# Kernel tuning notes

Measured on AMD Instinct MI355X. Metric: run time of the kernel, lower is better.

The kernel has to match this reference:

```python
import jax, jax.numpy as jnp
import numpy as np

B, T, IN, H, OUT = 512, 1024, 16, 128, 1


def _lstm_layer(x_tbd, W_ih, W_hh, b_ih, b_hh):
    """Single LSTM layer, PyTorch gate order (i, f, g, o).
    x_tbd: [T, B, D_in] -> returns [T, B, H]."""
    Tn, Bn = x_tbd.shape[0], x_tbd.shape[1]
    # Precompute input contribution for all timesteps: [T, B, 4H]
    gx = jnp.einsum('tbd,gd->tbg', x_tbd, W_ih) + b_ih + b_hh
    h0 = jnp.zeros((Bn, H), x_tbd.dtype)
    c0 = jnp.zeros((Bn, H), x_tbd.dtype)

    def step(carry, gx_t):
        h, c = carry
        gates = gx_t + h @ W_hh.T  # [B, 4H]
        i = jax.nn.sigmoid(gates[:, 0 * H:1 * H])
        f = jax.nn.sigmoid(gates[:, 1 * H:2 * H])
        g = jnp.tanh(gates[:, 2 * H:3 * H])
        o = jax.nn.sigmoid(gates[:, 3 * H:4 * H])
        c = f * c + i * g
        h = o * jnp.tanh(c)
        return (h, c), h

    _, hs = jax.lax.scan(step, (h0, c0), gx)
    return hs  # [T, B, H]


def setup_inputs() -> dict:
    key = jax.random.key(0)
    ks = jax.random.split(key, 12)
    s = 1.0 / np.sqrt(H)  # PyTorch LSTM init scale
    return {
        'x': jax.random.normal(ks[0], (B, T, IN), jnp.float32),
        'W_ih0': jax.random.uniform(ks[1], (4 * H, IN), jnp.float32, -s, s),
        'W_hh0': jax.random.uniform(ks[2], (4 * H, H), jnp.float32, -s, s),
        'b_ih0': jax.random.uniform(ks[3], (4 * H,), jnp.float32, -s, s),
        'b_hh0': jax.random.uniform(ks[4], (4 * H,), jnp.float32, -s, s),
        'W_ih1': jax.random.uniform(ks[5], (4 * H, H), jnp.float32, -s, s),
        'W_hh1': jax.random.uniform(ks[6], (4 * H, H), jnp.float32, -s, s),
        'b_ih1': jax.random.uniform(ks[7], (4 * H,), jnp.float32, -s, s),
        'b_hh1': jax.random.uniform(ks[8], (4 * H,), jnp.float32, -s, s),
        'W_fc': jax.random.uniform(ks[9], (OUT, H), jnp.float32, -s, s),
        'b_fc': jax.random.uniform(ks[10], (OUT,), jnp.float32, -s, s),
    }


def reference(x, W_ih0, W_hh0, b_ih0, b_hh0, W_ih1, W_hh1, b_ih1, b_hh1, W_fc, b_fc):
    x_tbd = jnp.transpose(x, (1, 0, 2))  # [T, B, IN]
    h1 = _lstm_layer(x_tbd, W_ih0, W_hh0, b_ih0, b_hh0)  # [T, B, H]
    h2 = _lstm_layer(h1, W_ih1, W_hh1, b_ih1, b_hh1)     # [T, B, H]
    out = jnp.transpose(h2, (1, 0, 2))  # [B, T, H]
    out = jax.nn.relu(out)
    out = out @ W_fc.T + b_fc  # [B, T, 1]
    out = jax.nn.relu(out)
    return out
```

## Files before the change

### kernel.cpp

```cpp
#include <hip/hip_runtime.h>

#define T_SEQ  1024
#define NBATCH 512
#define IN_DIM 16
#define HDIM   128
#define G4     (4 * HDIM)
#define TC     64
#define NCHUNK (T_SEQ / TC)
#define NWGH   128

typedef unsigned short ushort_t;
typedef __attribute__((ext_vector_type(8))) _Float16 f16x8;
typedef __attribute__((ext_vector_type(4))) float f32x4;

#define MFMA16(a, b, c) __builtin_amdgcn_mfma_f32_16x16x32_f16((a), (b), (c), 0, 0, 0)

__device__ __forceinline__ float sigf(float x) {
  return __builtin_amdgcn_rcpf(1.0f + __expf(-x));
}
__device__ __forceinline__ float tanhf_fast(float x) {
  return 1.0f - 2.0f * __builtin_amdgcn_rcpf(1.0f + __expf(2.0f * x));
}
__device__ __forceinline__ ushort_t f16_bits(float f) {
  const _Float16 h = (_Float16)f;
  return __builtin_bit_cast(unsigned short, h);
}
__device__ __forceinline__ void split_f16(float f, ushort_t* hi, ushort_t* lo) {
  const _Float16 h = (_Float16)f;
  *hi = __builtin_bit_cast(unsigned short, h);
  const _Float16 l = (_Float16)(f - (float)h);
  *lo = __builtin_bit_cast(unsigned short, l);
}
__device__ __forceinline__ void bar_lds() {
  asm volatile("s_waitcnt lgkmcnt(0)\n\ts_barrier" ::: "memory");
}

__global__ __launch_bounds__(256) void prep_weights(
    const float* __restrict__ Whh0, const float* __restrict__ Whh1,
    const float* __restrict__ Wih0, const float* __restrict__ Wih1,
    ushort_t* __restrict__ w0h, ushort_t* __restrict__ w0l,
    ushort_t* __restrict__ w1h, ushort_t* __restrict__ w1l,
    ushort_t* __restrict__ wxh, ushort_t* __restrict__ wxl,
    ushort_t* __restrict__ wi1h, ushort_t* __restrict__ wi1l)
{
  const int idx = blockIdx.x * 256 + threadIdx.x;
  if (idx < 512 * HDIM) {
    split_f16(Whh0[idx], &w0h[idx], &w0l[idx]);
    split_f16(Whh1[idx], &w1h[idx], &w1l[idx]);
    split_f16(Wih1[idx], &wi1h[idx], &wi1l[idx]);
  }
  if (idx < 512 * 32) {
    const int g = idx >> 5, k = idx & 31;
    const float f = (k < IN_DIM) ? Wih0[g * IN_DIM + k] : 0.0f;
    split_f16(f, &wxh[idx], &wxl[idx]);
  }
}

struct L0LDS {
  __align__(16) ushort_t hfA[4][144];
  __align__(16) ushort_t hfB[4][144];
  __align__(16) ushort_t xlds[4][TC][32];
  __align__(16) float gx0s[8 * 4 * 128 * 4];
};
struct L1LDS {
  __align__(16) ushort_t hfA[4][144];
  __align__(16) ushort_t hfB[4][144];
  __align__(16) ushort_t h2l[TC][4][136];
  __align__(16) float wfl[HDIM];
};

__global__ __launch_bounds__(512, 2) void lstm_pipe(
    const float* __restrict__ x,
    const ushort_t* __restrict__ w0h,
    const ushort_t* __restrict__ wxh, const ushort_t* __restrict__ wxl,
    const float* __restrict__ bih0, const float* __restrict__ bhh0,
    const ushort_t* __restrict__ wi1h,
    const ushort_t* __restrict__ w1h,
    const float* __restrict__ bih1, const float* __restrict__ bhh1,
    const float* __restrict__ Wfc, const float* __restrict__ bfc,
    float* __restrict__ out,
    float* __restrict__ h1s, float* __restrict__ c1s,
    float* __restrict__ h2s, float* __restrict__ c2s,
    ushort_t* __restrict__ h1buf,
    float* __restrict__ gx1buf,
    int ch)
{
  const int tid  = threadIdx.x;
  const int lane = tid & 63;
  const int wv   = tid >> 6;
  const int row  = lane & 15;
  const int kq   = lane >> 4;
  const int bq   = row >> 2;
  const int j    = wv * 16 + row;

  constexpr size_t POOL =
      sizeof(L0LDS) > sizeof(L1LDS) ? sizeof(L0LDS) : sizeof(L1LDS);
  __shared__ __align__(16) char pool[POOL];

  if (blockIdx.x < NWGH) {
    if (ch >= NCHUNK) return;
    L0LDS& S = *(L0LDS*)pool;
    const int w  = blockIdx.x;
    const int b0 = w * 4;

    f16x8 Bh[4][4], Bxh[4], Bxl[4];
#pragma unroll
    for (int i = 0; i < 4; ++i) {
      const int g = i * 128 + j;
#pragma unroll
      for (int kt = 0; kt < 4; ++kt)
        Bh[i][kt] = *(const f16x8*)&w0h[g * HDIM + kt * 32 + kq * 8];
      Bxh[i] = *(const f16x8*)&wxh[g * 32 + kq * 8];
      Bxl[i] = *(const f16x8*)&wxl[g * 32 + kq * 8];
    }

    {
      const int r = tid >> 1, half = tid & 1;
      const int b = r >> 6, ts = r & (TC - 1);
      const float* src =
          &x[((size_t)(b0 + b) * T_SEQ + ch * TC + ts) * IN_DIM + half * 8];
      const float4 v0 = *(const float4*)&src[0];
      const float4 v1 = *(const float4*)&src[4];
      ushort_t* dst = &S.xlds[b][ts][half * 8];
      dst[0] = f16_bits(v0.x); dst[1] = f16_bits(v0.y);
      dst[2] = f16_bits(v0.z); dst[3] = f16_bits(v0.w);
      dst[4] = f16_bits(v1.x); dst[5] = f16_bits(v1.y);
      dst[6] = f16_bits(v1.z); dst[7] = f16_bits(v1.w);
      *(float4*)&S.xlds[b][ts][16 + half * 8] = (float4){0.f, 0.f, 0.f, 0.f};
    }

    float bz[4];
#pragma unroll
    for (int i = 0; i < 4; ++i) bz[i] = bih0[i * 128 + j] + bhh0[i * 128 + j];
    float hc = h1s[(size_t)(b0 + kq) * HDIM + j];
    float cc = c1s[(size_t)(b0 + kq) * HDIM + j];
    S.hfA[kq][j] = f16_bits(hc);
    __syncthreads();

    ushort_t* hbp = h1buf + ((size_t)(ch & 1) * NWGH + w) * (TC * 4 * HDIM) +
                    (size_t)kq * HDIM + j;

#define L0_STEP(HIN, HOUT, TT)                                              \
  {                                                                         \
    const float4 zcu =                                                      \
        *(const float4*)&S.gx0s[((((TT) & 7) * 4 + kq) * 128 + j) * 4];     \
    f32x4 aH[4];                                                            \
    _Pragma("unroll") for (int i = 0; i < 4; ++i)                           \
        aH[i] = (f32x4){0.f, 0.f, 0.f, 0.f};                                \
    _Pragma("unroll") for (int kt = 0; kt < 4; ++kt) {                      \
      const f16x8 ah = *(const f16x8*)&S.HIN[bq][kt * 32 + kq * 8];         \
      _Pragma("unroll") for (int i = 0; i < 4; ++i)                         \
          aH[i] = MFMA16(ah, Bh[i][kt], aH[i]);                             \
    }                                                                       \
    const float ig = sigf(aH[0][0] + zcu.x);                                \
    const float fg = sigf(aH[1][0] + zcu.y);                                \
    const float gg = tanhf_fast(aH[2][0] + zcu.z);                          \
    const float og = sigf(aH[3][0] + zcu.w);                                \
    cc = fg * cc + ig * gg;                                                 \
    hc = og * tanhf_fast(cc);                                               \
    const ushort_t hbits = f16_bits(hc);                                    \
    S.HOUT[kq][j] = hbits;                                                  \
    *hbp = hbits;                                                           \
    hbp += 4 * HDIM;                                                        \
    bar_lds();                                                              \
  }

    for (int sc = 0; sc < TC / 8; ++sc) {
#pragma unroll
      for (int mt = 0; mt < 2; ++mt) {
        const f16x8 a =
            *(const f16x8*)&S.xlds[row & 3][sc * 8 + mt * 4 + (row >> 2)][kq * 8];
        f32x4 acc[4];
#pragma unroll
        for (int i = 0; i < 4; ++i) acc[i] = (f32x4){0.f, 0.f, 0.f, 0.f};
#pragma unroll
        for (int i = 0; i < 4; ++i) acc[i] = MFMA16(a, Bxh[i], acc[i]);
#pragma unroll
        for (int i = 0; i < 4; ++i) acc[i] = MFMA16(a, Bxl[i], acc[i]);
#pragma unroll
        for (int r = 0; r < 4; ++r) {
          float4 o;
          o.x = acc[0][r] + bz[0];
          o.y = acc[1][r] + bz[1];
          o.z = acc[2][r] + bz[2];
          o.w = acc[3][r] + bz[3];
          *(float4*)&S.gx0s[(((mt * 4 + kq) * 4 + r) * 128 + j) * 4] = o;
        }
      }
      bar_lds();
#pragma unroll 1
      for (int q = 0; q < 4; ++q) {
        const int tt = sc * 8 + q * 2;
        L0_STEP(hfA, hfB, tt);
        L0_STEP(hfB, hfA, tt + 1);
      }
    }
#undef L0_STEP

    h1s[(size_t)(b0 + kq) * HDIM + j] = hc;
    c1s[(size_t)(b0 + kq) * HDIM + j] = cc;
  } else {
    if (ch == 0) return;
    L1LDS& S = *(L1LDS*)pool;
    const int w  = blockIdx.x - NWGH;
    const int b0 = w * 4;

    const ushort_t* hb =
        h1buf + ((size_t)((ch - 1) & 1) * NWGH + w) * (TC * 4 * HDIM);
    float* gx = gx1buf + (size_t)w * (TC * 4 * HDIM * 4);

    if (tid < HDIM) S.wfl[tid] = Wfc[tid];

    {
      f16x8 Gh[4][4];
      float bz1[4];
#pragma unroll
      for (int i = 0; i < 4; ++i) {
        const int g = i * 128 + j;
#pragma unroll
        for (int kt = 0; kt < 4; ++kt)
          Gh[i][kt] = *(const f16x8*)&wi1h[g * HDIM + kt * 32 + kq * 8];
        bz1[i] = bih1[i * 128 + j] + bhh1[i * 128 + j];
      }
#pragma unroll 2
      for (int mt = 0; mt < TC * 4 / 16; ++mt) {
        f32x4 acc[4];
#pragma unroll
        for (int i = 0; i < 4; ++i) acc[i] = (f32x4){0.f, 0.f, 0.f, 0.f};
#pragma unroll
        for (int kt = 0; kt < 4; ++kt) {
          const f16x8 a =
              *(const f16x8*)&hb[(size_t)(mt * 16 + row) * HDIM + kt * 32 + kq * 8];
#pragma unroll
          for (int i = 0; i < 4; ++i) acc[i] = MFMA16(a, Gh[i][kt], acc[i]);
        }
#pragma unroll
        for (int r = 0; r < 4; ++r) {
          const int m = mt * 16 + kq * 4 + r;
          float4 o;
          o.x = acc[0][r] + bz1[0];
          o.y = acc[1][r] + bz1[1];
          o.z = acc[2][r] + bz1[2];
          o.w = acc[3][r] + bz1[3];
          *(float4*)&gx[((size_t)m * HDIM + j) * 4] = o;
        }
      }
    }

    float hc = h2s[(size_t)(b0 + kq) * HDIM + j];
    float cc = c2s[(size_t)(b0 + kq) * HDIM + j];
    S.hfA[kq][j] = f16_bits(hc);
    __syncthreads();

    f16x8 Rh[4][4];
#pragma unroll
    for (int i = 0; i < 4; ++i) {
      const int g = i * 128 + j;
#pragma unroll
      for (int kt = 0; kt < 4; ++kt)
        Rh[i][kt] = *(const f16x8*)&w1h[g * HDIM + kt * 32 + kq * 8];
    }

    const float4* gxp = (const float4*)&gx[((size_t)kq * HDIM + j) * 4];
    float4 zcc = *gxp;
    gxp += 512;

#define L1_STEP(HIN, HOUT, TT)                                              \
  {                                                                         \
    const float4 zcu = zcc;                                                 \
    if ((TT) + 1 < TC) { zcc = *gxp; gxp += 512; }                          \
    f32x4 aH[4];                                                            \
    _Pragma("unroll") for (int i = 0; i < 4; ++i)                           \
        aH[i] = (f32x4){0.f, 0.f, 0.f, 0.f};                                \
    _Pragma("unroll") for (int kt = 0; kt < 4; ++kt) {                      \
      const f16x8 ah = *(const f16x8*)&S.HIN[bq][kt * 32 + kq * 8];         \
      _Pragma("unroll") for (int i = 0; i < 4; ++i)                         \
          aH[i] = MFMA16(ah, Rh[i][kt], aH[i]);                             \
    }                                                                       \
    const float ig = sigf(aH[0][0] + zcu.x);                                \
    const float fg = sigf(aH[1][0] + zcu.y);                                \
    const float gg = tanhf_fast(aH[2][0] + zcu.z);                          \
    const float og = sigf(aH[3][0] + zcu.w);                                \
    cc = fg * cc + ig * gg;                                                 \
    hc = og * tanhf_fast(cc);                                               \
    const ushort_t hbits = f16_bits(hc);                                    \
    S.HOUT[kq][j] = hbits;                                                  \
    S.h2l[TT][kq][j] = hbits;                                               \
    bar_lds();                                                              \
  }

    for (int tt = 0; tt < TC; tt += 2) {
      L1_STEP(hfA, hfB, tt);
      L1_STEP(hfB, hfA, tt + 1);
    }
#undef L1_STEP

    h2s[(size_t)(b0 + kq) * HDIM + j] = hc;
    c2s[(size_t)(b0 + kq) * HDIM + j] = cc;

    if (tid < TC * 4) {
      const int tt = tid >> 2, b = tid & 3;
      const float bfcv = bfc[0];
      float s0 = 0.f, s1 = 0.f, s2 = 0.f, s3 = 0.f;
#pragma unroll
      for (int q = 0; q < HDIM / 8; ++q) {
        const f16x8 hv = *(const f16x8*)&S.h2l[tt][b][q * 8];
        const float* wq = &S.wfl[q * 8];
        s0 += fmaxf((float)hv[0], 0.f) * wq[0];
        s1 += fmaxf((float)hv[1], 0.f) * wq[1];
        s2 += fmaxf((float)hv[2], 0.f) * wq[2];
        s3 += fmaxf((float)hv[3], 0.f) * wq[3];
        s0 += fmaxf((float)hv[4], 0.f) * wq[4];
        s1 += fmaxf((float)hv[5], 0.f) * wq[5];
        s2 += fmaxf((float)hv[6], 0.f) * wq[6];
        s3 += fmaxf((float)hv[7], 0.f) * wq[7];
      }
      const float s = s0 + s1 + s2 + s3 + bfcv;
      out[(size_t)(b0 + b) * T_SEQ + (ch - 1) * TC + tt] = fmaxf(s, 0.0f);
    }
  }
}

extern "C" void kernel_launch(void* const* d_in, const int* in_sizes, int n_in,
                              void* d_out, int out_size, void* d_ws, size_t ws_size,
                              hipStream_t stream)
{
  const float* x    = (const float*)d_in[0];
  const float* Wih0 = (const float*)d_in[1];
  const float* Whh0 = (const float*)d_in[2];
  const float* bih0 = (const float*)d_in[3];
  const float* bhh0 = (const float*)d_in[4];
  const float* Wih1 = (const float*)d_in[5];
  const float* Whh1 = (const float*)d_in[6];
  const float* bih1 = (const float*)d_in[7];
  const float* bhh1 = (const float*)d_in[8];
  const float* Wfc  = (const float*)d_in[9];
  const float* bfc  = (const float*)d_in[10];
  float* out = (float*)d_out;

  const size_t stateN = (size_t)NBATCH * HDIM;
  float* h1s = (float*)d_ws;
  float* c1s = h1s + stateN;
  float* h2s = c1s + stateN;
  float* c2s = h2s + stateN;
  ushort_t* w0h  = (ushort_t*)(c2s + stateN);
  ushort_t* w0l  = w0h  + stateN;
  ushort_t* w1h  = w0l  + stateN;
  ushort_t* w1l  = w1h  + stateN;
  ushort_t* wi1h = w1l  + stateN;
  ushort_t* wi1l = wi1h + stateN;
  ushort_t* wxh  = wi1l + stateN;
  ushort_t* wxl  = wxh  + 512 * 32;
  ushort_t* h1buf = wxl + 512 * 32;
  float* gx1buf = (float*)(h1buf + (size_t)2 * NWGH * TC * 4 * HDIM);

  (void)hipMemsetAsync(d_ws, 0, 4 * stateN * sizeof(float), stream);
  hipLaunchKernelGGL(prep_weights, dim3(256), dim3(256), 0, stream,
                     Whh0, Whh1, Wih0, Wih1,
                     w0h, w0l, w1h, w1l, wxh, wxl, wi1h, wi1l);

  for (int ch = 0; ch <= NCHUNK; ++ch) {
    hipLaunchKernelGGL(lstm_pipe, dim3(2 * NWGH), dim3(512), 0, stream,
                       x, w0h, wxh, wxl, bih0, bhh0,
                       wi1h, w1h, bih1, bhh1, Wfc, bfc,
                       out, h1s, c1s, h2s, c2s, h1buf, gx1buf, ch);
  }
}
```

Before: 926.7 us.

## Interleave layer-1 input projection with recurrence via LDS instead of a global gx buffer

Layer 1 no longer precomputes the input projection for the whole chunk into a global fp32 buffer. It now computes it four timesteps at a time into a small padded LDS tile, right before the recurrent steps that use it, reloading the wi1h weights from global or cache each sub-chunk. The h2 outputs go to a global fp16 buffer instead of LDS, and the FC epilogue reads them back after a barrier. The layer-0 x-projection weights are also reloaded per sub-chunk to cut register pressure. This removes the large global gx round trip and spreads the projection work between recurrent steps, at the cost of repeated weight loads and an extra barrier per sub-chunk.

```diff
diff --git a/kernel.cpp b/kernel.cpp
--- a/kernel.cpp
+++ b/kernel.cpp
@@ -56,6 +56,8 @@
   }
 }
 
+#define GXS 516
+
 struct L0LDS {
   __align__(16) ushort_t hfA[4][144];
   __align__(16) ushort_t hfB[4][144];
@@ -65,7 +67,7 @@
 struct L1LDS {
   __align__(16) ushort_t hfA[4][144];
   __align__(16) ushort_t hfB[4][144];
-  __align__(16) ushort_t h2l[TC][4][136];
+  __align__(16) float gxs[16 * GXS];
   __align__(16) float wfl[HDIM];
 };
 
@@ -82,7 +84,7 @@
     float* __restrict__ h1s, float* __restrict__ c1s,
     float* __restrict__ h2s, float* __restrict__ c2s,
     ushort_t* __restrict__ h1buf,
-    float* __restrict__ gx1buf,
+    ushort_t* __restrict__ h2buf,
     int ch)
 {
   const int tid  = threadIdx.x;
@@ -103,15 +105,13 @@
     const int w  = blockIdx.x;
     const int b0 = w * 4;
 
-    f16x8 Bh[4][4], Bxh[4], Bxl[4];
+    f16x8 Bh[4][4];
 #pragma unroll
     for (int i = 0; i < 4; ++i) {
       const int g = i * 128 + j;
 #pragma unroll
       for (int kt = 0; kt < 4; ++kt)
         Bh[i][kt] = *(const f16x8*)&w0h[g * HDIM + kt * 32 + kq * 8];
-      Bxh[i] = *(const f16x8*)&wxh[g * 32 + kq * 8];
-      Bxl[i] = *(const f16x8*)&wxl[g * 32 + kq * 8];
     }
 
     {
@@ -148,7 +148,7 @@
     _Pragma("unroll") for (int i = 0; i < 4; ++i)                           \
         aH[i] = (f32x4){0.f, 0.f, 0.f, 0.f};                                \
     _Pragma("unroll") for (int kt = 0; kt < 4; ++kt) {                      \
-      const f16x8 ah = *(const f16x8*)&S.HIN[bq][kt * 32 + kq * 8];         \
+      const f16x8 ah = *(const f16x8*)&HIN[bq][kt * 32 + kq * 8];           \
       _Pragma("unroll") for (int i = 0; i < 4; ++i)                         \
           aH[i] = MFMA16(ah, Bh[i][kt], aH[i]);                             \
     }                                                                       \
@@ -159,40 +159,49 @@
     cc = fg * cc + ig * gg;                                                 \
     hc = og * tanhf_fast(cc);                                               \
     const ushort_t hbits = f16_bits(hc);                                    \
-    S.HOUT[kq][j] = hbits;                                                  \
+    HOUT[kq][j] = hbits;                                                    \
     *hbp = hbits;                                                           \
     hbp += 4 * HDIM;                                                        \
     bar_lds();                                                              \
   }
 
     for (int sc = 0; sc < TC / 8; ++sc) {
-#pragma unroll
-      for (int mt = 0; mt < 2; ++mt) {
-        const f16x8 a =
-            *(const f16x8*)&S.xlds[row & 3][sc * 8 + mt * 4 + (row >> 2)][kq * 8];
-        f32x4 acc[4];
-#pragma unroll
-        for (int i = 0; i < 4; ++i) acc[i] = (f32x4){0.f, 0.f, 0.f, 0.f};
-#pragma unroll
-        for (int i = 0; i < 4; ++i) acc[i] = MFMA16(a, Bxh[i], acc[i]);
-#pragma unroll
-        for (int i = 0; i < 4; ++i) acc[i] = MFMA16(a, Bxl[i], acc[i]);
-#pragma unroll
-        for (int r = 0; r < 4; ++r) {
-          float4 o;
-          o.x = acc[0][r] + bz[0];
-          o.y = acc[1][r] + bz[1];
-          o.z = acc[2][r] + bz[2];
-          o.w = acc[3][r] + bz[3];
-          *(float4*)&S.gx0s[(((mt * 4 + kq) * 4 + r) * 128 + j) * 4] = o;
+      {
+        f16x8 Bxh[4], Bxl[4];
+#pragma unroll
+        for (int i = 0; i < 4; ++i) {
+          const int g = i * 128 + j;
+          Bxh[i] = *(const f16x8*)&wxh[g * 32 + kq * 8];
+          Bxl[i] = *(const f16x8*)&wxl[g * 32 + kq * 8];
+        }
+#pragma unroll
+        for (int mt = 0; mt < 2; ++mt) {
+          const f16x8 a = *(const f16x8*)
+              &S.xlds[row & 3][sc * 8 + mt * 4 + (row >> 2)][kq * 8];
+          f32x4 acc[4];
+#pragma unroll
+          for (int i = 0; i < 4; ++i) acc[i] = (f32x4){0.f, 0.f, 0.f, 0.f};
+#pragma unroll
+          for (int i = 0; i < 4; ++i) acc[i] = MFMA16(a, Bxh[i], acc[i]);
+#pragma unroll
+          for (int i = 0; i < 4; ++i) acc[i] = MFMA16(a, Bxl[i], acc[i]);
+#pragma unroll
+          for (int r = 0; r < 4; ++r) {
+            float4 o;
+            o.x = acc[0][r] + bz[0];
+            o.y = acc[1][r] + bz[1];
+            o.z = acc[2][r] + bz[2];
+            o.w = acc[3][r] + bz[3];
+            *(float4*)&S.gx0s[(((mt * 4 + kq) * 4 + r) * 128 + j) * 4] = o;
+          }
         }
       }
-      bar_lds();
+      __syncthreads();
 #pragma unroll 1
       for (int q = 0; q < 4; ++q) {
         const int tt = sc * 8 + q * 2;
-        L0_STEP(hfA, hfB, tt);
-        L0_STEP(hfB, hfA, tt + 1);
+        L0_STEP(S.hfA, S.hfB, tt);
+        L0_STEP(S.hfB, S.hfA, tt + 1);
       }
     }
 #undef L0_STEP
@@ -207,44 +216,21 @@
 
     const ushort_t* hb =
         h1buf + ((size_t)((ch - 1) & 1) * NWGH + w) * (TC * 4 * HDIM);
-    float* gx = gx1buf + (size_t)w * (TC * 4 * HDIM * 4);
+    ushort_t* h2p = h2buf + (size_t)w * (TC * 4 * HDIM) +
+                    (size_t)kq * HDIM + j;
 
     if (tid < HDIM) S.wfl[tid] = Wfc[tid];
 
-    {
-      f16x8 Gh[4][4];
-      float bz1[4];
-#pragma unroll
-      for (int i = 0; i < 4; ++i) {
-        const int g = i * 128 + j;
-#pragma unroll
-        for (int kt = 0; kt < 4; ++kt)
-          Gh[i][kt] = *(const f16x8*)&wi1h[g * HDIM + kt * 32 + kq * 8];
-        bz1[i] = bih1[i * 128 + j] + bhh1[i * 128 + j];
-      }
-#pragma unroll 2
-      for (int mt = 0; mt < TC * 4 / 16; ++mt) {
-        f32x4 acc[4];
-#pragma unroll
-        for (int i = 0; i < 4; ++i) acc[i] = (f32x4){0.f, 0.f, 0.f, 0.f};
-#pragma unroll
-        for (int kt = 0; kt < 4; ++kt) {
-          const f16x8 a =
-              *(const f16x8*)&hb[(size_t)(mt * 16 + row) * HDIM + kt * 32 + kq * 8];
-#pragma unroll
-          for (int i = 0; i < 4; ++i) acc[i] = MFMA16(a, Gh[i][kt], acc[i]);
-        }
-#pragma unroll
-        for (int r = 0; r < 4; ++r) {
-          const int m = mt * 16 + kq * 4 + r;
-          float4 o;
-          o.x = acc[0][r] + bz1[0];
-          o.y = acc[1][r] + bz1[1];
-          o.z = acc[2][r] + bz1[2];
-          o.w = acc[3][r] + bz1[3];
-          *(float4*)&gx[((size_t)m * HDIM + j) * 4] = o;
-        }
-      }
+    float bz1[4];
+#pragma unroll
+    for (int i = 0; i < 4; ++i) bz1[i] = bih1[i * 128 + j] + bhh1[i * 128 + j];
+    f16x8 Rh[4][4];
+#pragma unroll
+    for (int i = 0; i < 4; ++i) {
+      const int g = i * 128 + j;
+#pragma unroll
+      for (int kt = 0; kt < 4; ++kt)
+        Rh[i][kt] = *(const f16x8*)&w1h[g * HDIM + kt * 32 + kq * 8];
     }
 
     float hc = h2s[(size_t)(b0 + kq) * HDIM + j];
@@ -252,28 +238,15 @@
     S.hfA[kq][j] = f16_bits(hc);
     __syncthreads();
 
-    f16x8 Rh[4][4];
-#pragma unroll
-    for (int i = 0; i < 4; ++i) {
-      const int g = i * 128 + j;
-#pragma unroll
-      for (int kt = 0; kt < 4; ++kt)
-        Rh[i][kt] = *(const f16x8*)&w1h[g * HDIM + kt * 32 + kq * 8];
-    }
-
-    const float4* gxp = (const float4*)&gx[((size_t)kq * HDIM + j) * 4];
-    float4 zcc = *gxp;
-    gxp += 512;
-
 #define L1_STEP(HIN, HOUT, TT)                                              \
   {                                                                         \
-    const float4 zcu = zcc;                                                 \
-    if ((TT) + 1 < TC) { zcc = *gxp; gxp += 512; }                          \
+    const float4 zcu =                                                      \
+        *(const float4*)&S.gxs[((((TT) & 3) * 4 + kq)) * GXS + j * 4];      \
     f32x4 aH[4];                                                            \
     _Pragma("unroll") for (int i = 0; i < 4; ++i)                           \
         aH[i] = (f32x4){0.f, 0.f, 0.f, 0.f};                                \
     _Pragma("unroll") for (int kt = 0; kt < 4; ++kt) {                      \
-      const f16x8 ah = *(const f16x8*)&S.HIN[bq][kt * 32 + kq * 8];         \
+      const f16x8 ah = *(const f16x8*)&HIN[bq][kt * 32 + kq * 8];           \
       _Pragma("unroll") for (int i = 0; i < 4; ++i)                         \
           aH[i] = MFMA16(ah, Rh[i][kt], aH[i]);                             \
     }                                                                       \
@@ -284,27 +257,63 @@
     cc = fg * cc + ig * gg;                                                 \
     hc = og * tanhf_fast(cc);                                               \
     const ushort_t hbits = f16_bits(hc);                                    \
-    S.HOUT[kq][j] = hbits;                                                  \
-    S.h2l[TT][kq][j] = hbits;                                               \
+    HOUT[kq][j] = hbits;                                                    \
+    h2p[0] = hbits;                                                         \
+    h2p += 4 * HDIM;                                                        \
     bar_lds();                                                              \
   }
 
-    for (int tt = 0; tt < TC; tt += 2) {
-      L1_STEP(hfA, hfB, tt);
-      L1_STEP(hfB, hfA, tt + 1);
+    for (int sc = 0; sc < TC / 4; ++sc) {
+#pragma unroll
+      for (int half = 0; half < 2; ++half) {
+        f16x8 Gh[2][4];
+#pragma unroll
+        for (int i2 = 0; i2 < 2; ++i2) {
+          const int g = (half * 2 + i2) * 128 + j;
+#pragma unroll
+          for (int kt = 0; kt < 4; ++kt)
+            Gh[i2][kt] = *(const f16x8*)&wi1h[g * HDIM + kt * 32 + kq * 8];
+        }
+        f32x4 acc[2];
+        acc[0] = (f32x4){0.f, 0.f, 0.f, 0.f};
+        acc[1] = (f32x4){0.f, 0.f, 0.f, 0.f};
+#pragma unroll
+        for (int kt = 0; kt < 4; ++kt) {
+          const f16x8 a =
+              *(const f16x8*)&hb[(size_t)(sc * 16 + row) * HDIM + kt * 32 + kq * 8];
+          acc[0] = MFMA16(a, Gh[0][kt], acc[0]);
+          acc[1] = MFMA16(a, Gh[1][kt], acc[1]);
+        }
+#pragma unroll
+        for (int r = 0; r < 4; ++r) {
+          float2 o;
+          o.x = acc[0][r] + bz1[half * 2];
+          o.y = acc[1][r] + bz1[half * 2 + 1];
+          *(float2*)&S.gxs[(kq * 4 + r) * GXS + j * 4 + half * 2] = o;
+        }
+      }
+      bar_lds();
+      const int t0s = sc * 4;
+      L1_STEP(S.hfA, S.hfB, t0s);
+      L1_STEP(S.hfB, S.hfA, t0s + 1);
+      L1_STEP(S.hfA, S.hfB, t0s + 2);
+      L1_STEP(S.hfB, S.hfA, t0s + 3);
     }
 #undef L1_STEP
 
     h2s[(size_t)(b0 + kq) * HDIM + j] = hc;
     c2s[(size_t)(b0 + kq) * HDIM + j] = cc;
+    __syncthreads();
 
     if (tid < TC * 4) {
       const int tt = tid >> 2, b = tid & 3;
+      const ushort_t* hrow =
+          h2buf + (size_t)w * (TC * 4 * HDIM) + (size_t)tid * HDIM;
       const float bfcv = bfc[0];
       float s0 = 0.f, s1 = 0.f, s2 = 0.f, s3 = 0.f;
 #pragma unroll
       for (int q = 0; q < HDIM / 8; ++q) {
-        const f16x8 hv = *(const f16x8*)&S.h2l[tt][b][q * 8];
+        const f16x8 hv = *(const f16x8*)&hrow[q * 8];
         const float* wq = &S.wfl[q * 8];
         s0 += fmaxf((float)hv[0], 0.f) * wq[0];
         s1 += fmaxf((float)hv[1], 0.f) * wq[1];
@@ -352,7 +361,7 @@
   ushort_t* wxh  = wi1l + stateN;
   ushort_t* wxl  = wxh  + 512 * 32;
   ushort_t* h1buf = wxl + 512 * 32;
-  float* gx1buf = (float*)(h1buf + (size_t)2 * NWGH * TC * 4 * HDIM);
+  ushort_t* h2buf = h1buf + (size_t)2 * NWGH * TC * 4 * HDIM;
 
   (void)hipMemsetAsync(d_ws, 0, 4 * stateN * sizeof(float), stream);
   hipLaunchKernelGGL(prep_weights, dim3(256), dim3(256), 0, stream,
@@ -363,6 +372,6 @@
     hipLaunchKernelGGL(lstm_pipe, dim3(2 * NWGH), dim3(512), 0, stream,
                        x, w0h, wxh, wxl, bih0, bhh0,
                        wi1h, w1h, bih1, bhh1, Wfc, bfc,
-                       out, h1s, c1s, h2s, c2s, h1buf, gx1buf, ch);
-  }
-}
+                       out, h1s, c1s, h2s, c2s, h1buf, h2buf, ch);
+  }
+}
```

After: 958.9 us. 3.5% more time.
